# Kernel tuning notes

Hardware: AMD Instinct MI355X
Metric: run time of the kernel (lower is better)

Reference implementation:

```python
import jax, jax.numpy as jnp
import numpy as np

B, T, C, H = 4, 4096, 1024, 64

def setup_inputs() -> dict:
    key = jax.random.key(0)
    kx, kk, kq, kv = jax.random.split(key, 4)
    x = jax.random.normal(kx, (B, T, C), dtype=jnp.float32)
    # causal lower-triangular mask; masked_fill where mask == 0
    mask = jnp.tril(jnp.ones((T, T), dtype=jnp.int32))
    s = 1.0 / np.sqrt(C)
    Wk = jax.random.normal(kk, (H, C), dtype=jnp.float32) * s
    Wq = jax.random.normal(kq, (H, C), dtype=jnp.float32) * s
    Wv = jax.random.normal(kv, (H, C), dtype=jnp.float32) * s
    return {"x": x, "mask": mask, "Wk": Wk, "Wq": Wq, "Wv": Wv}

def reference(x, mask, Wk, Wq, Wv):
    # single-head attention; dropout is identity in eval mode
    scale = Wk.shape[0] ** -0.5  # head_size ** -0.5
    k = jnp.einsum('btc,hc->bth', x, Wk)  # [B,T,H]
    q = jnp.einsum('btc,hc->bth', x, Wq)
    v = jnp.einsum('btc,hc->bth', x, Wv)
    att = jnp.einsum('bqh,bkh->bqk', q, k) * scale  # [B,T,T]
    att = jnp.where(mask == 0, -jnp.inf, att)
    att = jax.nn.softmax(att, axis=-1)
    out = jnp.einsum('bqk,bkh->bqh', att, v)  # [B,T,H]
    return out
```

## Files before the change

### kernel.cpp

```cpp
#include <hip/hip_runtime.h>
#include <hip/hip_bf16.h>

#define BT 16384
#define CDIM 1024
#define HD 64
#define TT 4096

typedef __bf16 bf16x8 __attribute__((ext_vector_type(8)));
typedef __bf16 bf16x4 __attribute__((ext_vector_type(4)));
typedef float f32x4 __attribute__((ext_vector_type(4)));

__device__ __forceinline__ f32x4 mfma16(bf16x8 a, bf16x8 b, f32x4 c){
  return __builtin_amdgcn_mfma_f32_16x16x32_bf16(a, b, c, 0, 0, 0);
}

__global__ __launch_bounds__(256) void wconv_k(const float* __restrict__ Wk,
    const float* __restrict__ Wq, const float* __restrict__ Wv,
    __bf16* __restrict__ Wbf){
  int idx = blockIdx.x*256 + threadIdx.x;
  int e0 = idx*4;
  int n = e0 >> 10;
  int c = e0 & 1023;
  const float* src; float s;
  if (n < 64)      { src = Wk + (size_t)n*CDIM;       s = 1.0f;   }
  else if (n < 128){ src = Wq + (size_t)(n-64)*CDIM;  s = 0.125f; }
  else             { src = Wv + (size_t)(n-128)*CDIM; s = 1.0f;   }
  float4 v = *reinterpret_cast<const float4*>(src + c);
  __bf16* dst = Wbf + e0;
  dst[0]=(__bf16)(v.x*s); dst[1]=(__bf16)(v.y*s);
  dst[2]=(__bf16)(v.z*s); dst[3]=(__bf16)(v.w*s);
}

__global__ __launch_bounds__(512) void proj_k(const float* __restrict__ x,
    const __bf16* __restrict__ Wbf, __bf16* __restrict__ kb,
    __bf16* __restrict__ qb, __bf16* __restrict__ vTb){
  __shared__ __bf16 Wt[2][192][68];
  __shared__ __bf16 Xt[2][32][68];

  const int tid  = threadIdx.x;
  const int lane = tid & 63;
  const int w    = tid >> 6;
  const int wr   = w >> 2;
  const int wn   = w & 3;
  const int l15  = lane & 15, g = lane >> 4;
  const long row0 = (long)blockIdx.x*32;

  const int wrw0 = tid>>3, wrw1 = (tid+512)>>3, wrw2 = (tid+1024)>>3;
  const int wc8  = (tid & 7)*8;
  const int xrw  = tid >> 4, xc4 = (tid & 15)*4;

  const float*  xsrc = x + (row0 + xrw)*CDIM + xc4;
  const __bf16* ws0  = Wbf + (size_t)wrw0*CDIM + wc8;
  const __bf16* ws1  = Wbf + (size_t)wrw1*CDIM + wc8;
  const __bf16* ws2  = Wbf + (size_t)wrw2*CDIM + wc8;

  f32x4 acc[3];
  #pragma unroll
  for (int j=0;j<3;j++) acc[j] = (f32x4)(0.0f);

  bf16x8 w0, w1, w2; float4 xr;

  w0 = *reinterpret_cast<const bf16x8*>(ws0);
  w1 = *reinterpret_cast<const bf16x8*>(ws1);
  w2 = *reinterpret_cast<const bf16x8*>(ws2);
  xr = *reinterpret_cast<const float4*>(xsrc);
  *reinterpret_cast<bf16x8*>(&Wt[0][wrw0][wc8]) = w0;
  *reinterpret_cast<bf16x8*>(&Wt[0][wrw1][wc8]) = w1;
  *reinterpret_cast<bf16x8*>(&Wt[0][wrw2][wc8]) = w2;
  {
    bf16x4 xv;
    xv[0]=(__bf16)xr.x; xv[1]=(__bf16)xr.y; xv[2]=(__bf16)xr.z; xv[3]=(__bf16)xr.w;
    *reinterpret_cast<bf16x4*>(&Xt[0][xrw][xc4]) = xv;
  }
  w0 = *reinterpret_cast<const bf16x8*>(ws0 + 64);
  w1 = *reinterpret_cast<const bf16x8*>(ws1 + 64);
  w2 = *reinterpret_cast<const bf16x8*>(ws2 + 64);
  xr = *reinterpret_cast<const float4*>(xsrc + 64);
  __syncthreads();

  #pragma unroll 2
  for (int t=0; t<16; ++t){
    const int cur = t & 1, nxt = cur ^ 1;

    if (t+1 < 16){
      *reinterpret_cast<bf16x8*>(&Wt[nxt][wrw0][wc8]) = w0;
      *reinterpret_cast<bf16x8*>(&Wt[nxt][wrw1][wc8]) = w1;
      *reinterpret_cast<bf16x8*>(&Wt[nxt][wrw2][wc8]) = w2;
      bf16x4 xv;
      xv[0]=(__bf16)xr.x; xv[1]=(__bf16)xr.y; xv[2]=(__bf16)xr.z; xv[3]=(__bf16)xr.w;
      *reinterpret_cast<bf16x4*>(&Xt[nxt][xrw][xc4]) = xv;
    }
    if (t+2 < 16){
      const int nk0 = (t+2)*64;
      w0 = *reinterpret_cast<const bf16x8*>(ws0 + nk0);
      w1 = *reinterpret_cast<const bf16x8*>(ws1 + nk0);
      w2 = *reinterpret_cast<const bf16x8*>(ws2 + nk0);
      xr = *reinterpret_cast<const float4*>(xsrc + nk0);
    }
    {
      bf16x8 a0 = *reinterpret_cast<const bf16x8*>(&Xt[cur][wr*16 + l15][g*8]);
      bf16x8 a1 = *reinterpret_cast<const bf16x8*>(&Xt[cur][wr*16 + l15][g*8 + 32]);
      bf16x8 b0[3], b1[3];
      #pragma unroll
      for (int nf=0;nf<3;nf++){
        b0[nf] = *reinterpret_cast<const bf16x8*>(&Wt[cur][wn*48 + nf*16 + l15][g*8]);
        b1[nf] = *reinterpret_cast<const bf16x8*>(&Wt[cur][wn*48 + nf*16 + l15][g*8 + 32]);
      }
      #pragma unroll
      for (int nf=0;nf<3;nf++)
        acc[nf] = mfma16(a1, b1[nf], mfma16(a0, b0[nf], acc[nf]));
    }
    __syncthreads();
  }

  const long bidx = row0 >> 12;
  #pragma unroll
  for (int nf=0;nf<3;nf++){
    const int n0  = wn*48 + nf*16 + l15;
    const int mat = n0 >> 6;
    const int h   = n0 & 63;
    const long rbase = row0 + wr*16 + g*4;
    if (mat == 0){
      #pragma unroll
      for (int r=0;r<4;r++) kb[(rbase+r)*HD + h] = (__bf16)acc[nf][r];
    } else if (mat == 1){
      #pragma unroll
      for (int r=0;r<4;r++) qb[(rbase+r)*HD + h] = (__bf16)acc[nf][r];
    } else {
      bf16x4 t4;
      #pragma unroll
      for (int r=0;r<4;r++) t4[r] = (__bf16)acc[nf][r];
      *reinterpret_cast<bf16x4*>(vTb + (bidx*64 + h)*TT + (rbase & 4095)) = t4;
    }
  }
}

template<int NS>
__global__ __launch_bounds__(256) void attn_part_k(const __bf16* __restrict__ kbg,
    const __bf16* __restrict__ qbg, const __bf16* __restrict__ vT,
    __bf16* __restrict__ po, float* __restrict__ pl){
  __shared__ __bf16 Klds[64][68];
  __shared__ __bf16 Vlds[64][68];
  __shared__ __bf16 Plds[4][16][68];

  const int tid  = threadIdx.x;
  const int lane = tid & 63;
  const int w    = tid >> 6;
  const int l15  = lane & 15, g = lane >> 4;

  const int bi  = blockIdx.x;
  const int b   = bi / (64*NS);
  const int rem = bi % (64*NS);
  const int qt  = 63 - rem / NS;
  const int s   = rem % NS;

  const int ntiles = qt + 1;
  const int lo = ( s      * ntiles) / NS;
  const int hi = ((s + 1) * ntiles) / NS;
  const int pidx = (b*64 + qt)*NS + s;

  if (lo == hi){
    if (l15 == 0){
      #pragma unroll
      for (int r=0;r<4;r++) pl[pidx*64 + w*16 + g*4 + r] = 0.0f;
    }
    return;
  }

  const long qbase = (long)b*TT + (long)qt*64;

  bf16x8 qf0, qf1;
  {
    const __bf16* src = qbg + (qbase + w*16 + l15)*HD + g*8;
    qf0 = *reinterpret_cast<const bf16x8*>(src);
    qf1 = *reinterpret_cast<const bf16x8*>(src + 32);
  }

  f32x4 o[4];
  #pragma unroll
  for (int ch=0; ch<4; ++ch) o[ch] = (f32x4)(0.0f);
  float lp[4] = {0.f, 0.f, 0.f, 0.f};

  const __bf16* vbase = vT + (size_t)b*64*TT;

  const int skey = tid >> 2;
  const int sd0  = (tid & 3) * 16;
  bf16x8 kr0, kr1, vr0, vr1;

  {
    const long kvbase = (long)b*TT + (long)lo*64;
    const __bf16* ks = kbg + (kvbase + skey)*HD + sd0;
    kr0 = *reinterpret_cast<const bf16x8*>(ks);
    kr1 = *reinterpret_cast<const bf16x8*>(ks+8);
    const __bf16* vs = vbase + (size_t)skey*TT + lo*64 + sd0;
    vr0 = *reinterpret_cast<const bf16x8*>(vs);
    vr1 = *reinterpret_cast<const bf16x8*>(vs+8);
  }

  for (int kv=lo; kv<hi; ++kv){
    __syncthreads();
    *reinterpret_cast<bf16x8*>(&Klds[skey][sd0])   = kr0;
    *reinterpret_cast<bf16x8*>(&Klds[skey][sd0+8]) = kr1;
    *reinterpret_cast<bf16x8*>(&Vlds[skey][sd0])   = vr0;
    *reinterpret_cast<bf16x8*>(&Vlds[skey][sd0+8]) = vr1;
    __syncthreads();

    if (kv+1 < hi){
      const long nbase = (long)b*TT + (long)(kv+1)*64;
      const __bf16* ks = kbg + (nbase + skey)*HD + sd0;
      kr0 = *reinterpret_cast<const bf16x8*>(ks);
      kr1 = *reinterpret_cast<const bf16x8*>(ks+8);
      const __bf16* vs = vbase + (size_t)skey*TT + (kv+1)*64 + sd0;
      vr0 = *reinterpret_cast<const bf16x8*>(vs);
      vr1 = *reinterpret_cast<const bf16x8*>(vs+8);
    }

    f32x4 sv[4];
    __builtin_amdgcn_s_setprio(1);
    #pragma unroll
    for (int c=0;c<4;c++){
      bf16x8 kb0 = *reinterpret_cast<const bf16x8*>(&Klds[c*16 + l15][g*8]);
      bf16x8 kb1 = *reinterpret_cast<const bf16x8*>(&Klds[c*16 + l15][g*8 + 32]);
      sv[c] = mfma16(qf0, kb0, (f32x4)(-16.0f));
      sv[c] = mfma16(qf1, kb1, sv[c]);
    }
    __builtin_amdgcn_s_setprio(0);

    if (kv == qt){
      #pragma unroll
      for (int c=0;c<4;c++){
        const int key = c*16 + l15;
        #pragma unroll
        for (int r=0;r<4;r++){
          const int qr = w*16 + g*4 + r;
          if (key > qr) sv[c][r] = -1e30f;
        }
      }
    }

    #pragma unroll
    for (int c=0;c<4;c++){
      #pragma unroll
      for (int r=0;r<4;r++) sv[c][r] = __expf(sv[c][r]);
    }
    #pragma unroll
    for (int r=0;r<4;r++)
      lp[r] += (sv[0][r] + sv[1][r]) + (sv[2][r] + sv[3][r]);

    #pragma unroll
    for (int c=0;c<4;c++){
      #pragma unroll
      for (int r=0;r<4;r++) Plds[w][g*4+r][c*16 + l15] = (__bf16)sv[c][r];
    }
    asm volatile("s_waitcnt lgkmcnt(0)" ::: "memory");
    __builtin_amdgcn_sched_barrier(0);
    bf16x8 pa0 = *reinterpret_cast<const bf16x8*>(&Plds[w][l15][g*8]);
    bf16x8 pa1 = *reinterpret_cast<const bf16x8*>(&Plds[w][l15][g*8 + 32]);

    __builtin_amdgcn_s_setprio(1);
    #pragma unroll
    for (int ch=0; ch<4; ++ch){
      bf16x8 vb0 = *reinterpret_cast<const bf16x8*>(&Vlds[ch*16 + l15][g*8]);
      bf16x8 vb1 = *reinterpret_cast<const bf16x8*>(&Vlds[ch*16 + l15][g*8 + 32]);
      o[ch] = mfma16(pa0, vb0, o[ch]);
      o[ch] = mfma16(pa1, vb1, o[ch]);
    }
    __builtin_amdgcn_s_setprio(0);
  }

  float lr[4];
  #pragma unroll
  for (int r=0;r<4;r++){
    float v = lp[r];
    v += __shfl_xor(v, 1);
    v += __shfl_xor(v, 2);
    v += __shfl_xor(v, 4);
    v += __shfl_xor(v, 8);
    lr[r] = v;
  }
  float rl[4];
  #pragma unroll
  for (int r=0;r<4;r++) rl[r] = (lr[r] > 0.0f) ? 1.0f/lr[r] : 0.0f;

  __bf16* podst = po + (size_t)pidx*4096;
  #pragma unroll
  for (int ch=0; ch<4; ++ch){
    #pragma unroll
    for (int r=0;r<4;r++)
      podst[(w*16 + g*4 + r)*64 + ch*16 + l15] = (__bf16)(o[ch][r] * rl[r]);
  }
  if (l15 == 0){
    #pragma unroll
    for (int r=0;r<4;r++) pl[pidx*64 + w*16 + g*4 + r] = lr[r];
  }
}

template<int NS>
__global__ __launch_bounds__(256) void comb_k(const __bf16* __restrict__ po,
    const float* __restrict__ pl, float* __restrict__ out){
  const int idx4  = (blockIdx.x*256 + threadIdx.x)*4;
  const int qrow  = idx4 >> 6;
  const int dim0  = idx4 & 63;
  const int qtg   = qrow >> 6;
  const int rowin = qrow & 63;

  float num0=0.f, num1=0.f, num2=0.f, num3=0.f, den=0.f;
  #pragma unroll
  for (int s=0;s<NS;s++){
    const float lv = pl[(qtg*NS + s)*64 + rowin];
    den += lv;
    bf16x4 p4 = *reinterpret_cast<const bf16x4*>(
        po + (size_t)(qtg*NS + s)*4096 + rowin*64 + dim0);
    num0 += lv*(float)p4[0]; num1 += lv*(float)p4[1];
    num2 += lv*(float)p4[2]; num3 += lv*(float)p4[3];
  }
  const float rd = 1.0f/den;
  float4 o = make_float4(num0*rd, num1*rd, num2*rd, num3*rd);
  *reinterpret_cast<float4*>(out + idx4) = o;
}

extern "C" void kernel_launch(void* const* d_in, const int* in_sizes, int n_in,
                              void* d_out, int out_size, void* d_ws, size_t ws_size,
                              hipStream_t stream) {
  const float* x  = (const float*)d_in[0];
  const float* Wk = (const float*)d_in[2];
  const float* Wq = (const float*)d_in[3];
  const float* Wv = (const float*)d_in[4];
  float* out = (float*)d_out;

  char* ws = (char*)d_ws;
  __bf16* Wbf = (__bf16*)ws;
  __bf16* kb  = (__bf16*)(ws + 393216);
  __bf16* qb  = (__bf16*)(ws + 2490368);
  __bf16* vTb = (__bf16*)(ws + 4587520);
  __bf16* po  = (__bf16*)(ws + 6684672);

  wconv_k<<<192, 256, 0, stream>>>(Wk, Wq, Wv, Wbf);
  proj_k <<<512, 512, 0, stream>>>(x, Wbf, kb, qb, vTb);

  const size_t need8 = 6684672ull + (size_t)2048*4096*2 + (size_t)2048*64*4;
  if (ws_size >= need8){
    float* pl = (float*)(ws + 6684672 + (size_t)2048*4096*2);
    attn_part_k<8><<<2048, 256, 0, stream>>>(kb, qb, vTb, po, pl);
    comb_k<8>    <<<1024, 256, 0, stream>>>(po, pl, out);
  } else {
    float* pl = (float*)(ws + 6684672 + (size_t)1024*4096*2);
    attn_part_k<4><<<1024, 256, 0, stream>>>(kb, qb, vTb, po, pl);
    comb_k<4>    <<<1024, 256, 0, stream>>>(po, pl, out);
  }
}
```

Baseline: 59.89 us.

## Shrink projection tiles to 16 rows and drop LDS double buffering

The projection kernel now handles 16 rows per block with 256 threads, launching 1024 blocks instead of 512 blocks of 512 threads. The double-buffered shared-memory pipeline is replaced by a single buffer, with a register prefetch of the next slice issued after the barrier. The aim is more blocks across CUs and less LDS per block to raise occupancy. In exchange, each block reloads the full weight tile for only 16 rows, so weight traffic per output row doubles, and the two barriers per step expose more latency.

```diff
diff --git a/kernel.cpp b/kernel.cpp
--- a/kernel.cpp
+++ b/kernel.cpp
@@ -31,84 +31,68 @@
   dst[2]=(__bf16)(v.z*s); dst[3]=(__bf16)(v.w*s);
 }
 
-__global__ __launch_bounds__(512) void proj_k(const float* __restrict__ x,
+__global__ __launch_bounds__(256) void proj_k(const float* __restrict__ x,
     const __bf16* __restrict__ Wbf, __bf16* __restrict__ kb,
     __bf16* __restrict__ qb, __bf16* __restrict__ vTb){
-  __shared__ __bf16 Wt[2][192][68];
-  __shared__ __bf16 Xt[2][32][68];
+  __shared__ __bf16 Wt[192][68];
+  __shared__ __bf16 Xt[16][68];
 
   const int tid  = threadIdx.x;
   const int lane = tid & 63;
   const int w    = tid >> 6;
-  const int wr   = w >> 2;
-  const int wn   = w & 3;
   const int l15  = lane & 15, g = lane >> 4;
-  const long row0 = (long)blockIdx.x*32;
-
-  const int wrw0 = tid>>3, wrw1 = (tid+512)>>3, wrw2 = (tid+1024)>>3;
-  const int wc8  = (tid & 7)*8;
-  const int xrw  = tid >> 4, xc4 = (tid & 15)*4;
-
-  const float*  xsrc = x + (row0 + xrw)*CDIM + xc4;
-  const __bf16* ws0  = Wbf + (size_t)wrw0*CDIM + wc8;
-  const __bf16* ws1  = Wbf + (size_t)wrw1*CDIM + wc8;
-  const __bf16* ws2  = Wbf + (size_t)wrw2*CDIM + wc8;
+  const long row0 = (long)blockIdx.x*16;
+
+  int wrw[6], wc8[6];
+  #pragma unroll
+  for (int i=0;i<6;i++){
+    const int c = tid + 256*i;
+    wrw[i] = c >> 3;
+    wc8[i] = (c & 7)*8;
+  }
+  const int xrw = tid >> 4, xc4 = (tid & 15)*4;
+  const float* xsrc = x + (row0 + xrw)*CDIM + xc4;
 
   f32x4 acc[3];
   #pragma unroll
   for (int j=0;j<3;j++) acc[j] = (f32x4)(0.0f);
 
-  bf16x8 w0, w1, w2; float4 xr;
-
-  w0 = *reinterpret_cast<const bf16x8*>(ws0);
-  w1 = *reinterpret_cast<const bf16x8*>(ws1);
-  w2 = *reinterpret_cast<const bf16x8*>(ws2);
+  bf16x8 wreg[6];
+  float4 xr;
+
+  #pragma unroll
+  for (int i=0;i<6;i++)
+    wreg[i] = *reinterpret_cast<const bf16x8*>(Wbf + (size_t)wrw[i]*CDIM + wc8[i]);
   xr = *reinterpret_cast<const float4*>(xsrc);
-  *reinterpret_cast<bf16x8*>(&Wt[0][wrw0][wc8]) = w0;
-  *reinterpret_cast<bf16x8*>(&Wt[0][wrw1][wc8]) = w1;
-  *reinterpret_cast<bf16x8*>(&Wt[0][wrw2][wc8]) = w2;
-  {
-    bf16x4 xv;
-    xv[0]=(__bf16)xr.x; xv[1]=(__bf16)xr.y; xv[2]=(__bf16)xr.z; xv[3]=(__bf16)xr.w;
-    *reinterpret_cast<bf16x4*>(&Xt[0][xrw][xc4]) = xv;
-  }
-  w0 = *reinterpret_cast<const bf16x8*>(ws0 + 64);
-  w1 = *reinterpret_cast<const bf16x8*>(ws1 + 64);
-  w2 = *reinterpret_cast<const bf16x8*>(ws2 + 64);
-  xr = *reinterpret_cast<const float4*>(xsrc + 64);
-  __syncthreads();
-
-  #pragma unroll 2
+
   for (int t=0; t<16; ++t){
-    const int cur = t & 1, nxt = cur ^ 1;
-
-    if (t+1 < 16){
-      *reinterpret_cast<bf16x8*>(&Wt[nxt][wrw0][wc8]) = w0;
-      *reinterpret_cast<bf16x8*>(&Wt[nxt][wrw1][wc8]) = w1;
-      *reinterpret_cast<bf16x8*>(&Wt[nxt][wrw2][wc8]) = w2;
+    #pragma unroll
+    for (int i=0;i<6;i++)
+      *reinterpret_cast<bf16x8*>(&Wt[wrw[i]][wc8[i]]) = wreg[i];
+    {
       bf16x4 xv;
       xv[0]=(__bf16)xr.x; xv[1]=(__bf16)xr.y; xv[2]=(__bf16)xr.z; xv[3]=(__bf16)xr.w;
-      *reinterpret_cast<bf16x4*>(&Xt[nxt][xrw][xc4]) = xv;
-    }
-    if (t+2 < 16){
-      const int nk0 = (t+2)*64;
-      w0 = *reinterpret_cast<const bf16x8*>(ws0 + nk0);
-      w1 = *reinterpret_cast<const bf16x8*>(ws1 + nk0);
-      w2 = *reinterpret_cast<const bf16x8*>(ws2 + nk0);
-      xr = *reinterpret_cast<const float4*>(xsrc + nk0);
-    }
+      *reinterpret_cast<bf16x4*>(&Xt[xrw][xc4]) = xv;
+    }
+    __syncthreads();
+
+    if (t+1 < 16){
+      const int nk = (t+1)*64;
+      #pragma unroll
+      for (int i=0;i<6;i++)
+        wreg[i] = *reinterpret_cast<const bf16x8*>(Wbf + (size_t)wrw[i]*CDIM + nk + wc8[i]);
+      xr = *reinterpret_cast<const float4*>(xsrc + nk);
+    }
+
     {
-      bf16x8 a0 = *reinterpret_cast<const bf16x8*>(&Xt[cur][wr*16 + l15][g*8]);
-      bf16x8 a1 = *reinterpret_cast<const bf16x8*>(&Xt[cur][wr*16 + l15][g*8 + 32]);
-      bf16x8 b0[3], b1[3];
+      bf16x8 a0 = *reinterpret_cast<const bf16x8*>(&Xt[l15][g*8]);
+      bf16x8 a1 = *reinterpret_cast<const bf16x8*>(&Xt[l15][g*8 + 32]);
       #pragma unroll
       for (int nf=0;nf<3;nf++){
-        b0[nf] = *reinterpret_cast<const bf16x8*>(&Wt[cur][wn*48 + nf*16 + l15][g*8]);
-        b1[nf] = *reinterpret_cast<const bf16x8*>(&Wt[cur][wn*48 + nf*16 + l15][g*8 + 32]);
+        bf16x8 b0 = *reinterpret_cast<const bf16x8*>(&Wt[w*48 + nf*16 + l15][g*8]);
+        bf16x8 b1 = *reinterpret_cast<const bf16x8*>(&Wt[w*48 + nf*16 + l15][g*8 + 32]);
+        acc[nf] = mfma16(a1, b1, mfma16(a0, b0, acc[nf]));
       }
-      #pragma unroll
-      for (int nf=0;nf<3;nf++)
-        acc[nf] = mfma16(a1, b1[nf], mfma16(a0, b0[nf], acc[nf]));
     }
     __syncthreads();
   }
@@ -116,10 +100,10 @@
   const long bidx = row0 >> 12;
   #pragma unroll
   for (int nf=0;nf<3;nf++){
-    const int n0  = wn*48 + nf*16 + l15;
+    const int n0  = w*48 + nf*16 + l15;
     const int mat = n0 >> 6;
     const int h   = n0 & 63;
-    const long rbase = row0 + wr*16 + g*4;
+    const long rbase = row0 + g*4;
     if (mat == 0){
       #pragma unroll
       for (int r=0;r<4;r++) kb[(rbase+r)*HD + h] = (__bf16)acc[nf][r];
@@ -335,8 +319,8 @@
   __bf16* vTb = (__bf16*)(ws + 4587520);
   __bf16* po  = (__bf16*)(ws + 6684672);
 
-  wconv_k<<<192, 256, 0, stream>>>(Wk, Wq, Wv, Wbf);
-  proj_k <<<512, 512, 0, stream>>>(x, Wbf, kb, qb, vTb);
+  wconv_k<<<192,  256, 0, stream>>>(Wk, Wq, Wv, Wbf);
+  proj_k <<<1024, 256, 0, stream>>>(x, Wbf, kb, qb, vTb);
 
   const size_t need8 = 6684672ull + (size_t)2048*4096*2 + (size_t)2048*64*4;
   if (ws_size >= need8){
```

Result: slower. 66.92 us (+11.7%).
